# Kernel tuning notes

Hardware: AMD Instinct MI355X
Metric: run time of the kernel (lower is better)

Reference implementation:

```python
import jax, jax.numpy as jnp
import numpy as np
from jax import lax

LONG_EDGE = 1024
MAX_SIZE = 1333.0
STRIDES = (4, 8, 16, 32, 64)
SIZES = (32, 64, 128, 256, 512)
RATIOS = (0.5, 1.0, 2.0)
PRE_NMS_TOPK = 6000
POST_NMS_TOPK = 1000
NMS_THRESH = 0.7
NUM_CH = 256


def _gen_anchors_level(scale, ratios, shape, stride):
    # faithful copy of generate_anchors_keras (numpy, static)
    scales, ratios = np.meshgrid(np.array([scale], dtype=np.float64), np.array(ratios, dtype=np.float64))
    scales = scales.flatten(); ratios = ratios.flatten()
    size_ratios = stride * stride / ratios
    widths = np.round(np.sqrt(size_ratios))
    heights = np.round(widths * ratios)
    widths = widths * (scales / stride)
    heights = heights * (scales / stride)
    shifts_y = np.arange(0, shape[0]) * stride + (stride - 1) / 2
    shifts_x = np.arange(0, shape[1]) * stride + (stride - 1) / 2
    shifts_x, shifts_y = np.meshgrid(shifts_x, shifts_y)
    box_widths, box_centers_x = np.meshgrid(widths, shifts_x)
    box_heights, box_centers_y = np.meshgrid(heights, shifts_y)
    box_centers = np.stack([box_centers_y, box_centers_x], axis=2).reshape([-1, 2])
    box_sizes = np.stack([box_heights, box_widths], axis=2).reshape([-1, 2])
    boxes = np.concatenate([box_centers - 0.5 * (box_sizes - 1), box_centers + 0.5 * (box_sizes - 1)], axis=1)
    boxes[:, [2, 3]] += 1
    return boxes[:, [1, 0, 3, 2]].astype(np.float32)


def all_anchors():
    shapes = [(int(np.ceil(LONG_EDGE / s)),) * 2 for s in STRIDES]
    return np.concatenate([_gen_anchors_level(SIZES[i], RATIOS, shapes[i], STRIDES[i]) for i in range(len(STRIDES))], axis=0)


def conv2d(x, w, b, padding):
    y = lax.conv_general_dilated(x, w, (1, 1), padding, dimension_numbers=('NCHW', 'OIHW', 'NCHW'))
    return y + b[None, :, None, None]


def decode_bbox_target(deltas, anchors):
    # deltas, anchors: [K,4]
    txty, twth = deltas[:, :2], deltas[:, 2:]
    x1y1, x2y2 = anchors[:, :2], anchors[:, 2:]
    waha = x2y2 - x1y1
    xaya = (x2y2 + x1y1) * 0.5
    clipv = jnp.float32(np.log(MAX_SIZE / 16.0))
    wbhb = jnp.exp(jnp.minimum(twth, clipv)) * waha
    xbyb = txty * waha + xaya
    return jnp.concatenate([xbyb - wbhb * 0.5, xbyb + wbhb * 0.5], axis=1)


def clip_boxes(b, h, w):
    # faithful to source: x clamped to window[0]=h, y to window[1]=w
    return jnp.stack([b[:, 0].clip(0.0, h), b[:, 1].clip(0.0, w), b[:, 2].clip(0.0, h), b[:, 3].clip(0.0, w)], 1)


def nms_keep(boxes, thresh):
    # boxes sorted by descending score; greedy NMS over full IoU matrix
    x1, y1, x2, y2 = boxes[:, 0], boxes[:, 1], boxes[:, 2], boxes[:, 3]
    areas = (x2 - x1) * (y2 - y1)
    iw = jnp.clip(jnp.minimum(x2[:, None], x2[None, :]) - jnp.maximum(x1[:, None], x1[None, :]), 0.0)
    ih = jnp.clip(jnp.minimum(y2[:, None], y2[None, :]) - jnp.maximum(y1[:, None], y1[None, :]), 0.0)
    inter = iw * ih
    iou = inter / (areas[:, None] + areas[None, :] - inter)
    n = boxes.shape[0]
    sup = iou > thresh
    idxs = jnp.arange(n)
    def body(i, keep):
        row = sup[i] & (idxs > i)
        return jnp.where(keep[i], keep & ~row, keep)
    return lax.fori_loop(0, n, body, jnp.ones((n,), bool))


def rpn_forward(image, feats, w0, b0, wcls, bcls, wbox, bbox):
    labels, boxes_l = [], []
    for f in feats:
        hidden = jax.nn.relu(conv2d(f, w0, b0, 'SAME'))
        cls = conv2d(hidden, wcls, bcls, 'VALID')   # [1,A,H,W]
        box = conv2d(hidden, wbox, bbox, 'VALID')   # [1,4A,H,W]
        labels.append(jnp.transpose(cls, (0, 2, 3, 1)).reshape(1, -1, 1))
        boxes_l.append(jnp.transpose(box, (0, 2, 3, 1)).reshape(1, -1, 4))
    scores = jnp.concatenate(labels, axis=1)[0, :, 0]          # [N]
    box_logits = jnp.concatenate(boxes_l, axis=1)[0]           # [N,4]
    anchors = jnp.asarray(all_anchors())                       # [N,4]
    k = min(PRE_NMS_TOPK, anchors.shape[0])
    _, order = lax.top_k(scores, k)
    deltas = box_logits[order]
    pre_anch = anchors[order]
    dec = decode_bbox_target(deltas, pre_anch)
    h, w = float(image.shape[2]), float(image.shape[3])
    boxes = clip_boxes(dec, h, w)
    keep = nms_keep(lax.stop_gradient(boxes), NMS_THRESH)
    sel = jnp.argsort(~keep)[:POST_NMS_TOPK]  # stable: kept boxes in score order, then pad slots
    proposals = jnp.where(keep[sel][:, None], boxes[sel], 0.0)
    return proposals


def setup_inputs() -> dict:
    key = jax.random.key(0)
    ks = jax.random.split(key, 9)
    hw = [256, 128, 64, 32, 16]
    inp = {'image': jax.random.normal(ks[0], (1, 3, 1024, 1024), jnp.float32)}
    for i, s in enumerate(hw):
        inp[f'feat{i}'] = jax.random.normal(jax.random.fold_in(ks[1], i), (1, NUM_CH, s, s), jnp.float32)
    inp['w0'] = jax.random.normal(ks[2], (NUM_CH, NUM_CH, 3, 3), jnp.float32) * 0.01
    inp['b0'] = jnp.zeros((NUM_CH,), jnp.float32)
    inp['wcls'] = jax.random.normal(ks[3], (3, NUM_CH, 1, 1), jnp.float32) * 0.01
    inp['bcls'] = jnp.zeros((3,), jnp.float32)
    inp['wbox'] = jax.random.normal(ks[4], (12, NUM_CH, 1, 1), jnp.float32) * 0.01
    inp['bbox'] = jnp.zeros((12,), jnp.float32)
    return inp


def reference(image, feat0, feat1, feat2, feat3, feat4, w0, b0, wcls, bcls, wbox, bbox):
    feats = [feat0, feat1, feat2, feat3, feat4]
    return rpn_forward(image, feats, w0, b0, wcls, bcls, wbox, bbox)
```

## Files before the change

### kernel.cpp

```cpp
#include <hip/hip_runtime.h>
#include <cstdint>

typedef unsigned long long u64;
typedef unsigned int u32;
typedef unsigned short ushort;
typedef __attribute__((ext_vector_type(8))) short short8;
typedef __attribute__((ext_vector_type(4))) float f32x4;

#define A_TOTAL 261888
#define NPIX    87296
#define KTOP    6000
#define KTARGET 7800
#define NWORDS  94
#define CANDMAX 8192
#define PIXMAX  8192
#define NBINS   16384

__device__ __forceinline__ u64 score_key64(double s) {
  u64 u = (u64)__double_as_longlong(s);
  return (u & 0x8000000000000000ULL) ? ~u : (u | 0x8000000000000000ULL);
}
__device__ __forceinline__ u32 key32(float s) {
  u32 u = __float_as_uint(s);
  return (u & 0x80000000u) ? ~u : (u | 0x80000000u);
}
__device__ __forceinline__ ushort f2bf(float f) {
  u32 u = __float_as_uint(f);
  u32 r = (u + 0x7FFFu + ((u >> 16) & 1u)) >> 16;
  return (ushort)r;
}
__device__ __forceinline__ void pix_level(int pix, int& l, int& off) {
  if (pix < 65536)      { l = 0; off = 0; }
  else if (pix < 81920) { l = 1; off = 65536; }
  else if (pix < 86016) { l = 2; off = 81920; }
  else if (pix < 87040) { l = 3; off = 86016; }
  else                  { l = 4; off = 87040; }
}

__global__ void k_prep_w(const float* __restrict__ w0, float* __restrict__ wt,
                         ushort* __restrict__ wkf) {
  int i = blockIdx.x * 256 + threadIdx.x;
  if (i < 256 * 2304) {
    int o = i & 255;
    int ictap = i >> 8;
    float v = w0[o * 2304 + ictap];
    wt[ictap * 256 + o] = v;
    int ic = ictap / 9;
    int tap = ictap - ic * 9;
    int w = o >> 6, mt = (o >> 4) & 3, l15 = o & 15;
    int ch = ic >> 5, kk = ic & 31;
    int l4 = kk >> 3, e = kk & 7;
    int lane = l4 * 16 + l15;
    wkf[((((w * 4 + mt) * 8 + ch) * 9 + tap) << 9) + lane * 8 + e] = f2bf(v);
  }
}

__global__ __launch_bounds__(256, 2) void k_conv_mfma(
    const float* __restrict__ f0, const float* __restrict__ f1,
    const float* __restrict__ f2, const float* __restrict__ f3,
    const float* __restrict__ f4,
    const ushort* __restrict__ wkf, const float* __restrict__ b0,
    const float* __restrict__ wcls, const float* __restrict__ bcls,
    float* __restrict__ scr)
{
  __shared__ ushort xsl[100][40];
  __shared__ float  part[3][64][17];

  int b = blockIdx.x;
  int l, tb;
  if (b < 1024)      { l = 0; tb = b; }
  else if (b < 1280) { l = 1; tb = b - 1024; }
  else if (b < 1344) { l = 2; tb = b - 1280; }
  else if (b < 1360) { l = 3; tb = b - 1344; }
  else               { l = 4; tb = b - 1360; }
  const float* feat = (l == 0) ? f0 : (l == 1) ? f1 : (l == 2) ? f2 : (l == 3) ? f3 : f4;
  int Hh = 256 >> l;
  int HW = Hh * Hh;
  int pixOff = (l == 0) ? 0 : (l == 1) ? 65536 : (l == 2) ? 81920 : (l == 3) ? 86016 : 87040;
  int shl = 5 - l;
  int ty = (tb >> shl) << 3;
  int tx = (tb & ((1 << shl) - 1)) << 3;

  int tid = threadIdx.x;
  int w = tid >> 6;
  int lane = tid & 63;
  int l15 = lane & 15;
  int l4 = lane >> 4;

  f32x4 zz = {0.f, 0.f, 0.f, 0.f};
  f32x4 acc[4][4];
  #pragma unroll
  for (int mt = 0; mt < 4; ++mt)
    #pragma unroll
    for (int tt = 0; tt < 4; ++tt) acc[mt][tt] = zz;

  for (int ch = 0; ch < 8; ++ch) {
    __syncthreads();
    for (int e = tid; e < 3200; e += 256) {
      int icl = e / 100;
      int sp = e - icl * 100;
      int yy = sp / 10;
      int xx = sp - yy * 10;
      int gy = ty + yy - 1, gx = tx + xx - 1;
      float v = 0.f;
      if (gy >= 0 && gy < Hh && gx >= 0 && gx < Hh)
        v = feat[(ch * 32 + icl) * HW + gy * Hh + gx];
      xsl[sp][icl] = f2bf(v);
    }
    __syncthreads();
    #pragma unroll
    for (int tap = 0; tap < 9; ++tap) {
      int dy = tap / 3;
      int dx = tap - dy * 3;
      short8 af[4], bf[4];
      #pragma unroll
      for (int mt = 0; mt < 4; ++mt) {
        int abase = ((((w * 4 + mt) * 8 + ch) * 9 + tap) << 9) + (lane << 3);
        af[mt] = *(const short8*)(wkf + abase);
      }
      #pragma unroll
      for (int tt = 0; tt < 4; ++tt) {
        int p = (tt << 4) + l15;
        int sp = ((p >> 3) + dy) * 10 + (p & 7) + dx;
        bf[tt] = *(const short8*)&xsl[sp][l4 << 3];
      }
      #pragma unroll
      for (int mt = 0; mt < 4; ++mt)
        #pragma unroll
        for (int tt = 0; tt < 4; ++tt)
          acc[mt][tt] = __builtin_amdgcn_mfma_f32_16x16x32_bf16(af[mt], bf[tt], acc[mt][tt], 0, 0, 0);
    }
  }

  float pr[3][4];
  #pragma unroll
  for (int kk = 0; kk < 3; ++kk)
    #pragma unroll
    for (int tt = 0; tt < 4; ++tt) pr[kk][tt] = 0.f;
  #pragma unroll
  for (int mt = 0; mt < 4; ++mt) {
    #pragma unroll
    for (int r = 0; r < 4; ++r) {
      int oc = (w << 6) + (mt << 4) + (l4 << 2) + r;
      float bb = b0[oc];
      float c0 = wcls[oc], c1 = wcls[256 + oc], c2 = wcls[512 + oc];
      #pragma unroll
      for (int tt = 0; tt < 4; ++tt) {
        float v = acc[mt][tt][r] + bb;
        v = v > 0.f ? v : 0.f;
        pr[0][tt] = fmaf(c0, v, pr[0][tt]);
        pr[1][tt] = fmaf(c1, v, pr[1][tt]);
        pr[2][tt] = fmaf(c2, v, pr[2][tt]);
      }
    }
  }
  __syncthreads();
  #pragma unroll
  for (int kk = 0; kk < 3; ++kk)
    #pragma unroll
    for (int tt = 0; tt < 4; ++tt)
      part[kk][(tt << 4) + l15][(w << 2) + l4] = pr[kk][tt];
  __syncthreads();
  if (tid < 192) {
    int kk = tid >> 6;
    int px = tid & 63;
    float s = 0.f;
    #pragma unroll
    for (int q = 0; q < 16; ++q) s += part[kk][px][q];
    int pix = pixOff + (ty + (px >> 3)) * Hh + (tx + (px & 7));
    scr[pix * 3 + kk] = s + bcls[kk];
  }
}

__global__ void k_hist1(const float* __restrict__ scr, u32* __restrict__ bins) {
  __shared__ u32 h[NBINS];
  int tid = threadIdx.x;
  for (int idx = tid; idx < NBINS; idx += 256) h[idx] = 0;
  __syncthreads();
  for (int i = blockIdx.x * 256 + tid; i < A_TOTAL; i += gridDim.x * 256)
    atomicAdd(&h[key32(scr[i]) >> 18], 1u);
  __syncthreads();
  for (int idx = tid; idx < NBINS; idx += 256) {
    u32 v = h[idx];
    if (v) atomicAdd(&bins[idx], v);
  }
}

__global__ void k_scan1(const u32* __restrict__ bins, u32* __restrict__ meta) {
  __shared__ u32 psum[256];
  int tid = threadIdx.x;
  u32 s = 0;
  for (int u = 0; u < 64; ++u) s += bins[tid * 64 + u];
  psum[tid] = s;
  __syncthreads();
  if (tid == 0) {
    u32 run = 0;
    for (int t = 255; t >= 0; --t) { u32 tmp = psum[t]; psum[t] = run; run += tmp; }
  }
  __syncthreads();
  u32 cum = psum[tid];
  if (cum < (u32)KTARGET) {
    for (int u = 63; u >= 0; --u) {
      u32 bv = bins[tid * 64 + u];
      u32 nc = cum + bv;
      if (nc >= (u32)KTARGET) {
        meta[0] = (u32)(tid * 64 + u);
        meta[2] = cum;
        break;
      }
      cum = nc;
    }
  }
}

__global__ void k_hist2(const float* __restrict__ scr, const u32* __restrict__ meta,
                        u32* __restrict__ sub) {
  int i = blockIdx.x * 256 + threadIdx.x;
  if (i < A_TOTAL) {
    u32 k = key32(scr[i]);
    if ((k >> 18) == meta[0]) atomicAdd(&sub[(k >> 10) & 0xFFu], 1u);
  }
}

__global__ void k_scan2(const u32* __restrict__ sub, u32* __restrict__ meta) {
  if (threadIdx.x == 0) {
    u32 b = meta[0];
    u32 c = meta[2];
    u32 T = b << 18;
    for (int u = 255; u >= 0; --u) {
      c += sub[u];
      if (c >= (u32)KTARGET) { T = (b << 18) | ((u32)u << 10); break; }
    }
    meta[3] = (T >= (2u << 10)) ? (T - (2u << 10)) : 0u;
  }
}

__global__ void k_cnt(const float* __restrict__ scr, const u32* __restrict__ meta,
                      u32* __restrict__ blkCnt) {
  __shared__ u32 wc[4];
  int tid = threadIdx.x;
  int i = blockIdx.x * 256 + tid;
  bool q = (i < A_TOTAL) && (key32(scr[i]) >= meta[3]);
  u64 b = __ballot(q);
  if ((tid & 63) == 0) wc[tid >> 6] = (u32)__popcll(b);
  __syncthreads();
  if (tid == 0) blkCnt[blockIdx.x] = wc[0] + wc[1] + wc[2] + wc[3];
}

__global__ __launch_bounds__(1024) void k_scanblk(const u32* __restrict__ blkCnt,
                                                  u32* __restrict__ blkOff,
                                                  u32* __restrict__ totalOut) {
  __shared__ u32 buf[2][1024];
  int tid = threadIdx.x;
  u32 v = (tid < 1023) ? blkCnt[tid] : 0u;
  buf[0][tid] = v;
  __syncthreads();
  int src = 0;
  for (int d = 1; d < 1024; d <<= 1) {
    u32 t = buf[src][tid] + ((tid >= d) ? buf[src][tid - d] : 0u);
    buf[src ^ 1][tid] = t;
    src ^= 1;
    __syncthreads();
  }
  if (tid < 1023) blkOff[tid] = buf[src][tid] - v;
  if (tid == 0) totalOut[0] = buf[src][1022];
}

__global__ void k_fill(const float* __restrict__ scr, const u32* __restrict__ meta,
                       const u32* __restrict__ blkOff, u32* __restrict__ candIdx) {
  __shared__ u32 wbase[4];
  int tid = threadIdx.x;
  int lane = tid & 63, wv = tid >> 6;
  int i = blockIdx.x * 256 + tid;
  bool q = (i < A_TOTAL) && (key32(scr[i]) >= meta[3]);
  u64 b = __ballot(q);
  if (lane == 0) wbase[wv] = (u32)__popcll(b);
  __syncthreads();
  if (tid == 0) {
    u32 r = blkOff[blockIdx.x];
    #pragma unroll
    for (int w2 = 0; w2 < 4; ++w2) { u32 t = wbase[w2]; wbase[w2] = r; r += t; }
  }
  __syncthreads();
  if (q) {
    u32 rank = (u32)__popcll(b & ((1ULL << lane) - 1ULL));
    u32 pos = wbase[wv] + rank;
    if (pos < CANDMAX) candIdx[pos] = (u32)i;
  }
}

__global__ void k_cntP(const float* __restrict__ scr, const u32* __restrict__ meta,
                       u32* __restrict__ blkCntP) {
  __shared__ u32 wc[4];
  int tid = threadIdx.x;
  int p = blockIdx.x * 256 + tid;
  bool q = false;
  if (p < NPIX) {
    u32 T = meta[3];
    q = (key32(scr[p * 3 + 0]) >= T) || (key32(scr[p * 3 + 1]) >= T) || (key32(scr[p * 3 + 2]) >= T);
  }
  u64 b = __ballot(q);
  if ((tid & 63) == 0) wc[tid >> 6] = (u32)__popcll(b);
  __syncthreads();
  if (tid == 0) blkCntP[blockIdx.x] = wc[0] + wc[1] + wc[2] + wc[3];
}

__global__ void k_fillP(const float* __restrict__ scr, const u32* __restrict__ meta,
                        const u32* __restrict__ blkOffP,
                        u32* __restrict__ pixList, u32* __restrict__ pixMap) {
  __shared__ u32 wbase[4];
  int tid = threadIdx.x;
  int lane = tid & 63, wv = tid >> 6;
  int p = blockIdx.x * 256 + tid;
  bool q = false;
  if (p < NPIX) {
    u32 T = meta[3];
    q = (key32(scr[p * 3 + 0]) >= T) || (key32(scr[p * 3 + 1]) >= T) || (key32(scr[p * 3 + 2]) >= T);
  }
  u64 b = __ballot(q);
  if (lane == 0) wbase[wv] = (u32)__popcll(b);
  __syncthreads();
  if (tid == 0) {
    u32 r = blkOffP[blockIdx.x];
    #pragma unroll
    for (int w2 = 0; w2 < 4; ++w2) { u32 t = wbase[w2]; wbase[w2] = r; r += t; }
  }
  __syncthreads();
  if (q) {
    u32 rank = (u32)__popcll(b & ((1ULL << lane) - 1ULL));
    u32 pos = wbase[wv] + rank;
    if (pos < PIXMAX) { pixList[pos] = (u32)p; pixMap[p] = pos; }
  }
}

#define KC 576
__global__ __launch_bounds__(256, 4) void k_hidden(
    const float* __restrict__ f0, const float* __restrict__ f1,
    const float* __restrict__ f2, const float* __restrict__ f3,
    const float* __restrict__ f4,
    const float* __restrict__ wt, const float* __restrict__ b0,
    const u32* __restrict__ pixList, const u32* __restrict__ meta,
    double* __restrict__ hbuf)
{
  __shared__ __align__(16) float patch[2][KC][8];
  __shared__ int sValid[8], sY[8], sX[8], sW[8], sL[8];

  int tid = threadIdx.x;
  int base = blockIdx.x * 8;
  u32 np = meta[4];
  if (np > PIXMAX) np = PIXMAX;
  if (base >= (int)np) return;

  if (tid < 8) {
    int slot = base + tid;
    int v = slot < (int)np;
    sValid[tid] = v;
    int pix = v ? (int)pixList[slot] : 0;
    int l, off;
    pix_level(pix, l, off);
    int W = 256 >> l;
    int idx = pix - off;
    sL[tid] = l;
    sW[tid] = W;
    sY[tid] = idx >> (8 - l);
    sX[tid] = idx & (W - 1);
  }
  __syncthreads();

  auto stage = [&](int c, int pb) {
    for (int t = tid; t < 1536; t += 256) {
      int s = t / 192;
      int rem = t - s * 192;
      int icl = rem / 3;
      int dy = rem - icl * 3;
      int ic = c * 64 + icl;
      float v0 = 0.f, v1 = 0.f, v2 = 0.f;
      if (sValid[s]) {
        int l = sL[s], W = sW[s], y = sY[s], x = sX[s];
        const float* feat = (l == 0) ? f0 : (l == 1) ? f1 : (l == 2) ? f2 : (l == 3) ? f3 : f4;
        int gy = y + dy - 1;
        if (gy >= 0 && gy < W) {
          const float* rowp = feat + ic * W * W + gy * W;
          if (x - 1 >= 0) v0 = rowp[x - 1];
          v1 = rowp[x];
          if (x + 1 < W) v2 = rowp[x + 1];
        }
      }
      int kb = icl * 9 + dy * 3;
      patch[pb][kb + 0][s] = v0;
      patch[pb][kb + 1][s] = v1;
      patch[pb][kb + 2][s] = v2;
    }
  };

  stage(0, 0);
  __syncthreads();

  double h[8];
  #pragma unroll
  for (int s = 0; s < 8; ++s) h[s] = 0.0;

  for (int c = 0; c < 4; ++c) {
    if (c < 3) stage(c + 1, (c + 1) & 1);
    const float* wcol = wt + (c * KC) * 256 + tid;
    const float (*pc)[8] = patch[c & 1];
    for (int kk = 0; kk < KC; ++kk) {
      double wv_ = (double)wcol[(size_t)kk * 256];
      float4 pa = *(const float4*)&pc[kk][0];
      float4 pb2 = *(const float4*)&pc[kk][4];
      h[0] = fma(wv_, (double)pa.x, h[0]);
      h[1] = fma(wv_, (double)pa.y, h[1]);
      h[2] = fma(wv_, (double)pa.z, h[2]);
      h[3] = fma(wv_, (double)pa.w, h[3]);
      h[4] = fma(wv_, (double)pb2.x, h[4]);
      h[5] = fma(wv_, (double)pb2.y, h[5]);
      h[6] = fma(wv_, (double)pb2.z, h[6]);
      h[7] = fma(wv_, (double)pb2.w, h[7]);
    }
    __syncthreads();
  }

  double bb = (double)b0[tid];
  #pragma unroll
  for (int s = 0; s < 8; ++s) {
    if (sValid[s]) {
      double t = h[s] + bb;
      hbuf[(size_t)(base + s) * 256 + tid] = t > 0.0 ? t : 0.0;
    }
  }
}

__global__ __launch_bounds__(256, 4) void k_heads(
    const float* __restrict__ wcls, const float* __restrict__ bcls,
    const float* __restrict__ wbox, const float* __restrict__ bbox,
    const u32* __restrict__ candIdx, const u32* __restrict__ pixMap,
    const u32* __restrict__ meta, const double* __restrict__ hbuf,
    u64* __restrict__ candKey, u32* __restrict__ candPack, double* __restrict__ candDelta)
{
  __shared__ double wavePart[8][5][4];
  __shared__ int sIdx[8], sValid[8], sR[8], sPS[8];
  int tid = threadIdx.x;
  int lane = tid & 63;
  int wv = tid >> 6;
  int base = blockIdx.x * 8;
  u32 cnt = meta[1];
  if (cnt > CANDMAX) cnt = CANDMAX;

  if (base >= (int)cnt) {
    if (tid < 8) {
      candKey[base + tid] = 0ULL;
      candPack[base + tid] = 0xFFFFFFFFu;
    }
    return;
  }

  if (tid < 8) {
    int slot = base + tid;
    int v = slot < (int)cnt;
    sValid[tid] = v;
    int aidx = v ? (int)candIdx[slot] : 0;
    sIdx[tid] = aidx;
    int pix = aidx / 3;
    sR[tid] = aidx - pix * 3;
    sPS[tid] = v ? (int)pixMap[pix] : 0;
  }
  __syncthreads();

  for (int s = 0; s < 8; ++s) {
    if (!sValid[s]) continue;
    int r = sR[s];
    double hv = hbuf[(size_t)sPS[s] * 256 + tid];
    double p0 = (double)wcls[r * 256 + tid] * hv;
    double p1 = (double)wbox[(r * 4 + 0) * 256 + tid] * hv;
    double p2 = (double)wbox[(r * 4 + 1) * 256 + tid] * hv;
    double p3 = (double)wbox[(r * 4 + 2) * 256 + tid] * hv;
    double p4 = (double)wbox[(r * 4 + 3) * 256 + tid] * hv;
    #pragma unroll
    for (int d = 32; d; d >>= 1) {
      p0 += __shfl_xor(p0, d);
      p1 += __shfl_xor(p1, d);
      p2 += __shfl_xor(p2, d);
      p3 += __shfl_xor(p3, d);
      p4 += __shfl_xor(p4, d);
    }
    if (lane == 0) {
      wavePart[s][0][wv] = p0;
      wavePart[s][1][wv] = p1;
      wavePart[s][2][wv] = p2;
      wavePart[s][3][wv] = p3;
      wavePart[s][4][wv] = p4;
    }
  }
  __syncthreads();
  if (tid < 40) {
    int s = tid / 5;
    int k = tid - s * 5;
    int slot = base + s;
    if (sValid[s]) {
      double v = wavePart[s][k][0] + wavePart[s][k][1] + wavePart[s][k][2] + wavePart[s][k][3];
      int r = sR[s];
      if (k == 0) {
        double sc_ = v + (double)bcls[r];
        candKey[slot] = score_key64(sc_);
        candPack[slot] = ((u32)sIdx[s] << 13) | (u32)slot;
      } else {
        candDelta[(size_t)slot * 4 + (k - 1)] = v + (double)bbox[r * 4 + (k - 1)];
      }
    } else if (k == 0) {
      candKey[slot] = 0ULL;
      candPack[slot] = 0xFFFFFFFFu;
    }
  }
}

__global__ __launch_bounds__(256) void k_rank(const u64* __restrict__ candKey,
                                              const u32* __restrict__ candPack,
                                              u32* __restrict__ order) {
  __shared__ u64 fk[1024];
  __shared__ u32 fp[1024];
  __shared__ u32 rsum[32][8];
  int tid = threadIdx.x;
  int c = tid & 31;
  int g = tid >> 5;
  int ci = blockIdx.x * 32 + c;
  u64 mk = candKey[ci];
  u32 mp = candPack[ci];
  u32 cnt = 0;
  for (int chunk = 0; chunk < 8; ++chunk) {
    __syncthreads();
    for (int e = tid; e < 1024; e += 256) {
      fk[e] = candKey[chunk * 1024 + e];
      fp[e] = candPack[chunk * 1024 + e];
    }
    __syncthreads();
    int j0 = g * 128;
    #pragma unroll 4
    for (int j = j0; j < j0 + 128; ++j) {
      u64 kj = fk[j];
      cnt += (kj > mk || (kj == mk && fp[j] < mp)) ? 1u : 0u;
    }
  }
  rsum[c][g] = cnt;
  __syncthreads();
  if (tid < 32) {
    u32 rank = 0;
    #pragma unroll
    for (int q = 0; q < 8; ++q) rank += rsum[tid][q];
    if (rank < (u32)KTOP) order[rank] = mp;
  }
}

__global__ void k_decode(const u32* __restrict__ order, const double* __restrict__ candDelta,
                         double* __restrict__ boxesD) {
  int i = blockIdx.x * 64 + threadIdx.x;
  if (i >= KTOP) return;
  u32 pack = order[i];
  u32 slot = pack & 0x1FFFu;
  u32 a = pack >> 13;
  int pix = (int)(a / 3u);
  int r = (int)(a - (u32)pix * 3u);
  int l, off;
  pix_level(pix, l, off);
  int W = 256 >> l;
  int idx = pix - off;
  int y = idx >> (8 - l);
  int x = idx & (W - 1);
  int s = 4 << l;
  double ratio = (r == 0) ? 0.5 : (r == 1) ? 1.0 : 2.0;
  double wq = rint(sqrt((double)(s * s) / ratio));
  double hq = rint(wq * ratio);
  double Wa = wq * 8.0, Ha = hq * 8.0;
  double cx = (double)x * (double)s + (double)(s - 1) * 0.5;
  double cy = (double)y * (double)s + (double)(s - 1) * 0.5;
  double ax1 = (double)(float)(cx - 0.5 * (Wa - 1.0));
  double ay1 = (double)(float)(cy - 0.5 * (Ha - 1.0));
  double ax2 = (double)(float)(cx + 0.5 * (Wa - 1.0) + 1.0);
  double ay2 = (double)(float)(cy + 0.5 * (Ha - 1.0) + 1.0);
  double tx = candDelta[(size_t)slot * 4 + 0], tyv = candDelta[(size_t)slot * 4 + 1];
  double tw = candDelta[(size_t)slot * 4 + 2], th  = candDelta[(size_t)slot * 4 + 3];
  double wa = ax2 - ax1, ha = ay2 - ay1;
  double xa = (ax1 + ax2) * 0.5, ya = (ay1 + ay2) * 0.5;
  double clipv = (double)(float)log(1333.0 / 16.0);
  double wb = exp(fmin(tw, clipv)) * wa;
  double hb = exp(fmin(th, clipv)) * ha;
  double xb = tx * wa + xa;
  double yb = tyv * ha + ya;
  double bx1 = xb - 0.5 * wb, by1 = yb - 0.5 * hb;
  double bx2 = xb + 0.5 * wb, by2 = yb + 0.5 * hb;
  bx1 = fmin(fmax(bx1, 0.0), 1024.0);
  by1 = fmin(fmax(by1, 0.0), 1024.0);
  bx2 = fmin(fmax(bx2, 0.0), 1024.0);
  by2 = fmin(fmax(by2, 0.0), 1024.0);
  boxesD[(size_t)i * 4 + 0] = bx1;
  boxesD[(size_t)i * 4 + 1] = by1;
  boxesD[(size_t)i * 4 + 2] = bx2;
  boxesD[(size_t)i * 4 + 3] = by2;
}

__global__ void k_mask(const double* __restrict__ boxesD, u64* __restrict__ maskA) {
  __shared__ double cbx[64][4];
  int lane = threadIdx.x;
  int bc = blockIdx.x, br = blockIdx.y;
  if (bc < br) return;
  int ci = bc * 64 + lane;
  if (ci < KTOP) {
    cbx[lane][0] = boxesD[(size_t)ci * 4 + 0];
    cbx[lane][1] = boxesD[(size_t)ci * 4 + 1];
    cbx[lane][2] = boxesD[(size_t)ci * 4 + 2];
    cbx[lane][3] = boxesD[(size_t)ci * 4 + 3];
  } else {
    cbx[lane][0] = -1e30; cbx[lane][1] = -1e30; cbx[lane][2] = -1e30; cbx[lane][3] = -1e30;
  }
  __syncthreads();
  int ri = br * 64 + lane;
  if (ri >= KTOP) return;
  double rx1 = boxesD[(size_t)ri * 4 + 0], ry1 = boxesD[(size_t)ri * 4 + 1];
  double rx2 = boxesD[(size_t)ri * 4 + 2], ry2 = boxesD[(size_t)ri * 4 + 3];
  double ra = (rx2 - rx1) * (ry2 - ry1);
  u64 bits = 0;
  #pragma unroll 4
  for (int j = 0; j < 64; ++j) {
    int cj = bc * 64 + j;
    double iw = fmin(rx2, cbx[j][2]) - fmax(rx1, cbx[j][0]);
    double ih = fmin(ry2, cbx[j][3]) - fmax(ry1, cbx[j][1]);
    iw = fmax(iw, 0.0); ih = fmax(ih, 0.0);
    double inter = iw * ih;
    double ca = (cbx[j][2] - cbx[j][0]) * (cbx[j][3] - cbx[j][1]);
    double iou = inter / (ra + ca - inter);
    if (cj > ri && iou > 0.7) bits |= (1ULL << j);
  }
  maskA[(size_t)ri * NWORDS + bc] = bits;
}

__global__ __launch_bounds__(1024) void k_nms_reduce(const u64* __restrict__ maskA,
                                                     u32* __restrict__ keep) {
  __shared__ u64 rm[NWORDS];
  int tid = threadIdx.x;
  int wv = tid >> 6, lane = tid & 63;
  for (int i = tid; i < NWORDS; i += 1024) rm[i] = 0ULL;
  __syncthreads();
  u64 diagNext = maskA[(size_t)lane * NWORDS + 0];
  int keptTot = 0;
  for (int c = 0; c < NWORDS; ++c) {
    int rows = KTOP - c * 64; if (rows > 64) rows = 64;
    u64 validM = (rows == 64) ? ~0ULL : ((1ULL << rows) - 1ULL);
    size_t rowbase = (size_t)(c * 64 + lane) * NWORDS;
    bool lv = lane < rows;
    int w0i = c + wv;
    u64 v0 = (lv && w0i      < NWORDS) ? maskA[rowbase + w0i]      : 0ULL;
    u64 v1 = (lv && w0i + 16 < NWORDS) ? maskA[rowbase + w0i + 16] : 0ULL;
    u64 v2 = (lv && w0i + 32 < NWORDS) ? maskA[rowbase + w0i + 32] : 0ULL;
    u64 v3 = (lv && w0i + 48 < NWORDS) ? maskA[rowbase + w0i + 48] : 0ULL;
    u64 v4 = (lv && w0i + 64 < NWORDS) ? maskA[rowbase + w0i + 64] : 0ULL;
    u64 v5 = (lv && w0i + 80 < NWORDS) ? maskA[rowbase + w0i + 80] : 0ULL;
    u64 diag = diagNext;
    if (c + 1 < NWORDS) {
      int nrows = KTOP - (c + 1) * 64; if (nrows > 64) nrows = 64;
      diagNext = (lane < nrows) ? maskA[(size_t)((c + 1) * 64 + lane) * NWORDS + (c + 1)] : 0ULL;
    }
    u64 R = rm[c];
    u64 undec = (~R) & validM;
    u64 km = 0;
    while (undec) {
      int j = __builtin_ctzll(undec);
      km |= (1ULL << j);
      u64 dj = (u64)__shfl((unsigned long long)diag, j);
      undec &= ~(dj | (1ULL << j));
    }
    if (wv == 0 && lane < rows) keep[c * 64 + lane] = (u32)((km >> lane) & 1ULL);
    keptTot += (int)__popcll(km);
    if (keptTot >= 1000) {
      for (int i = (c + 1) * 64 + tid; i < KTOP; i += 1024) keep[i] = 0u;
      return;
    }
    u64 sel = ((km >> lane) & 1ULL) ? ~0ULL : 0ULL;
    v0 &= sel; v1 &= sel; v2 &= sel; v3 &= sel; v4 &= sel; v5 &= sel;
    #pragma unroll
    for (int s = 32; s; s >>= 1) {
      v0 |= (u64)__shfl_xor((unsigned long long)v0, s);
      v1 |= (u64)__shfl_xor((unsigned long long)v1, s);
      v2 |= (u64)__shfl_xor((unsigned long long)v2, s);
      v3 |= (u64)__shfl_xor((unsigned long long)v3, s);
      v4 |= (u64)__shfl_xor((unsigned long long)v4, s);
      v5 |= (u64)__shfl_xor((unsigned long long)v5, s);
    }
    if (lane == 0) {
      if (w0i      < NWORDS) rm[w0i]      |= v0;
      if (w0i + 16 < NWORDS) rm[w0i + 16] |= v1;
      if (w0i + 32 < NWORDS) rm[w0i + 32] |= v2;
      if (w0i + 48 < NWORDS) rm[w0i + 48] |= v3;
      if (w0i + 64 < NWORDS) rm[w0i + 64] |= v4;
      if (w0i + 80 < NWORDS) rm[w0i + 80] |= v5;
    }
    __syncthreads();
  }
}

__global__ __launch_bounds__(1024) void k_emit(const u32* __restrict__ keep,
                                               const double* __restrict__ boxesD,
                                               float* __restrict__ out) {
  __shared__ u32 partial[1024];
  __shared__ u32 excl[1024];
  int tid = threadIdx.x;
  for (int j = tid; j < 4000; j += 1024) out[j] = 0.f;
  int base = tid * 6;
  u32 kv[6];
  u32 c = 0;
  #pragma unroll
  for (int u = 0; u < 6; ++u) {
    int j = base + u;
    kv[u] = (j < KTOP) ? keep[j] : 0u;
    c += kv[u];
  }
  partial[tid] = c;
  __syncthreads();
  if (tid == 0) {
    u32 run = 0;
    for (int t = 0; t < 1024; ++t) { excl[t] = run; run += partial[t]; }
  }
  __syncthreads();
  u32 p = excl[tid];
  #pragma unroll
  for (int u = 0; u < 6; ++u) {
    int j = base + u;
    if (j < KTOP && kv[u]) {
      if (p < 1000u) {
        out[p * 4 + 0] = (float)boxesD[(size_t)j * 4 + 0];
        out[p * 4 + 1] = (float)boxesD[(size_t)j * 4 + 1];
        out[p * 4 + 2] = (float)boxesD[(size_t)j * 4 + 2];
        out[p * 4 + 3] = (float)boxesD[(size_t)j * 4 + 3];
      }
      ++p;
    }
  }
}

extern "C" void kernel_launch(void* const* d_in, const int* in_sizes, int n_in,
                              void* d_out, int out_size, void* d_ws, size_t ws_size,
                              hipStream_t stream) {
  const float* f0   = (const float*)d_in[1];
  const float* f1   = (const float*)d_in[2];
  const float* f2   = (const float*)d_in[3];
  const float* f3   = (const float*)d_in[4];
  const float* f4   = (const float*)d_in[5];
  const float* w0   = (const float*)d_in[6];
  const float* b0   = (const float*)d_in[7];
  const float* wcls = (const float*)d_in[8];
  const float* bcls = (const float*)d_in[9];
  const float* wbox = (const float*)d_in[10];
  const float* bbox = (const float*)d_in[11];
  float* out = (float*)d_out;
  char* ws = (char*)d_ws;

  size_t off = 0;
  auto alloc = [&](size_t bytes) { size_t o = off; off += (bytes + 255) & ~(size_t)255; return o; };
  size_t off_scr  = alloc((size_t)A_TOTAL * 4);
  size_t off_wt   = alloc((size_t)256 * 2304 * 4);
  size_t off_wk   = alloc((size_t)256 * 2304 * 2);
  size_t off_hb   = alloc((size_t)PIXMAX * 256 * 8);
  size_t off_ci   = alloc((size_t)CANDMAX * 4);
  size_t off_ck   = alloc((size_t)CANDMAX * 8);
  size_t off_cp   = alloc((size_t)CANDMAX * 4);
  size_t off_cd   = alloc((size_t)CANDMAX * 4 * 8);
  size_t off_pl   = alloc((size_t)PIXMAX * 4);
  size_t off_pm   = alloc((size_t)NPIX * 4);
  size_t off_box  = alloc((size_t)KTOP * 4 * 8);
  size_t off_ord  = alloc((size_t)KTOP * 4);
  size_t off_keep = alloc((size_t)KTOP * 4);
  size_t off_mask = alloc((size_t)KTOP * NWORDS * 8);
  size_t off_bcnt = alloc((size_t)1024 * 4);
  size_t off_boff = alloc((size_t)1024 * 4);
  size_t off_bcp  = alloc((size_t)1024 * 4);
  size_t off_bop  = alloc((size_t)1024 * 4);
  size_t off_bins = alloc((size_t)NBINS * 4);
  size_t off_sub  = alloc((size_t)256 * 4);
  size_t off_meta = alloc((size_t)64 * 4);
  size_t off_end  = off;
  (void)in_sizes; (void)n_in; (void)out_size; (void)ws_size;

  float*  scr       = (float*)(ws + off_scr);
  float*  wt        = (float*)(ws + off_wt);
  ushort* wkf       = (ushort*)(ws + off_wk);
  double* hbuf      = (double*)(ws + off_hb);
  u32*    candIdx   = (u32*)(ws + off_ci);
  u64*    candKey   = (u64*)(ws + off_ck);
  u32*    candPack  = (u32*)(ws + off_cp);
  double* candDelta = (double*)(ws + off_cd);
  u32*    pixList   = (u32*)(ws + off_pl);
  u32*    pixMap    = (u32*)(ws + off_pm);
  double* boxesD    = (double*)(ws + off_box);
  u32*    order     = (u32*)(ws + off_ord);
  u32*    keep      = (u32*)(ws + off_keep);
  u64*    maskA     = (u64*)(ws + off_mask);
  u32*    blkCnt    = (u32*)(ws + off_bcnt);
  u32*    blkOff    = (u32*)(ws + off_boff);
  u32*    blkCntP   = (u32*)(ws + off_bcp);
  u32*    blkOffP   = (u32*)(ws + off_bop);
  u32*    bins      = (u32*)(ws + off_bins);
  u32*    sub       = (u32*)(ws + off_sub);
  u32*    meta      = (u32*)(ws + off_meta);

  hipMemsetAsync(ws + off_bins, 0, off_end - off_bins, stream);

  k_prep_w<<<2304, 256, 0, stream>>>(w0, wt, wkf);
  k_conv_mfma<<<1364, 256, 0, stream>>>(f0, f1, f2, f3, f4, wkf, b0, wcls, bcls, scr);
  k_hist1<<<64, 256, 0, stream>>>(scr, bins);
  k_scan1<<<1, 256, 0, stream>>>(bins, meta);
  k_hist2<<<1023, 256, 0, stream>>>(scr, meta, sub);
  k_scan2<<<1, 64, 0, stream>>>(sub, meta);
  k_cnt<<<1023, 256, 0, stream>>>(scr, meta, blkCnt);
  k_scanblk<<<1, 1024, 0, stream>>>(blkCnt, blkOff, meta + 1);
  k_fill<<<1023, 256, 0, stream>>>(scr, meta, blkOff, candIdx);
  k_cntP<<<1023, 256, 0, stream>>>(scr, meta, blkCntP);
  k_scanblk<<<1, 1024, 0, stream>>>(blkCntP, blkOffP, meta + 4);
  k_fillP<<<1023, 256, 0, stream>>>(scr, meta, blkOffP, pixList, pixMap);
  k_hidden<<<PIXMAX / 8, 256, 0, stream>>>(f0, f1, f2, f3, f4, wt, b0, pixList, meta, hbuf);
  k_heads<<<CANDMAX / 8, 256, 0, stream>>>(wcls, bcls, wbox, bbox, candIdx, pixMap, meta, hbuf,
                                           candKey, candPack, candDelta);
  k_rank<<<CANDMAX / 32, 256, 0, stream>>>(candKey, candPack, order);
  k_decode<<<94, 64, 0, stream>>>(order, candDelta, boxesD);
  k_mask<<<dim3(NWORDS, NWORDS), 64, 0, stream>>>(boxesD, maskA);
  k_nms_reduce<<<1, 1024, 0, stream>>>(maskA, keep);
  k_emit<<<1, 1024, 0, stream>>>(keep, boxesD, out);
}
```

Baseline: 981.3 us.

## Recompute selected hidden pixels with FP64 MFMA and fuse compaction passes

```diff
diff --git a/kernel.cpp b/kernel.cpp
--- a/kernel.cpp
+++ b/kernel.cpp
@@ -6,6 +6,7 @@
 typedef unsigned short ushort;
 typedef __attribute__((ext_vector_type(8))) short short8;
 typedef __attribute__((ext_vector_type(4))) float f32x4;
+typedef __attribute__((ext_vector_type(4))) double f64x4;
 
 #define A_TOTAL 261888
 #define NPIX    87296
@@ -16,6 +17,15 @@
 #define PIXMAX  8192
 #define NBINS   16384
 
+#if defined(__has_builtin)
+#if __has_builtin(__builtin_amdgcn_mfma_f64_16x16x4f64)
+#define HAVE_DGEMM 1
+#endif
+#endif
+#ifndef HAVE_DGEMM
+#define HAVE_DGEMM 0
+#endif
+
 __device__ __forceinline__ u64 score_key64(double s) {
   u64 u = (u64)__double_as_longlong(s);
   return (u & 0x8000000000000000ULL) ? ~u : (u | 0x8000000000000000ULL);
@@ -37,14 +47,14 @@
   else                  { l = 4; off = 87040; }
 }
 
-__global__ void k_prep_w(const float* __restrict__ w0, float* __restrict__ wt,
+__global__ void k_prep_w(const float* __restrict__ w0, double* __restrict__ wt64,
                          ushort* __restrict__ wkf) {
   int i = blockIdx.x * 256 + threadIdx.x;
   if (i < 256 * 2304) {
     int o = i & 255;
     int ictap = i >> 8;
     float v = w0[o * 2304 + ictap];
-    wt[ictap * 256 + o] = v;
+    wt64[(size_t)ictap * 256 + o] = (double)v;
     int ic = ictap / 9;
     int tap = ictap - ic * 9;
     int w = o >> 6, mt = (o >> 4) & 3, l15 = o & 15;
@@ -53,6 +63,30 @@
     int lane = l4 * 16 + l15;
     wkf[((((w * 4 + mt) * 8 + ch) * 9 + tap) << 9) + lane * 8 + e] = f2bf(v);
   }
+}
+
+__global__ void k_probe(u32* __restrict__ flag) {
+#if HAVE_DGEMM
+  int l = threadIdx.x;
+  int m = l & 15, kq = l >> 4;
+  double a = (double)(1 + m * 4 + kq);
+  double b = (double)(1 + m * 4 + kq * 67);
+  f64x4 c = {0.0, 0.0, 0.0, 0.0};
+  c = __builtin_amdgcn_mfma_f64_16x16x4f64(a, b, c, 0, 0, 0);
+  bool ok = true;
+  #pragma unroll
+  for (int r = 0; r < 4; ++r) {
+    int row = 4 * kq + r, col = m;
+    double e = 0.0;
+    for (int k = 0; k < 4; ++k)
+      e += (double)(1 + row * 4 + k) * (double)(1 + col * 4 + k * 67);
+    if (c[r] != e) ok = false;
+  }
+  u64 bal = __ballot(ok);
+  if (l == 0) *flag = (bal == ~0ULL) ? 1u : 0u;
+#else
+  if (threadIdx.x == 0) *flag = 0u;
+#endif
 }
 
 __global__ __launch_bounds__(256, 2) void k_conv_mfma(
@@ -235,115 +269,203 @@
   }
 }
 
-__global__ void k_cnt(const float* __restrict__ scr, const u32* __restrict__ meta,
-                      u32* __restrict__ blkCnt) {
-  __shared__ u32 wc[4];
-  int tid = threadIdx.x;
+__global__ void k_cnt2(const float* __restrict__ scr, const u32* __restrict__ meta,
+                       u32* __restrict__ blkCnt, u32* __restrict__ blkCntP) {
+  __shared__ u32 wc[4], wcp[4];
+  int tid = threadIdx.x;
+  int lane = tid & 63, wv = tid >> 6;
+  u32 T = meta[3];
   int i = blockIdx.x * 256 + tid;
-  bool q = (i < A_TOTAL) && (key32(scr[i]) >= meta[3]);
-  u64 b = __ballot(q);
-  if ((tid & 63) == 0) wc[tid >> 6] = (u32)__popcll(b);
-  __syncthreads();
-  if (tid == 0) blkCnt[blockIdx.x] = wc[0] + wc[1] + wc[2] + wc[3];
-}
-
-__global__ __launch_bounds__(1024) void k_scanblk(const u32* __restrict__ blkCnt,
-                                                  u32* __restrict__ blkOff,
-                                                  u32* __restrict__ totalOut) {
+  bool qa = (i < A_TOTAL) && (key32(scr[i]) >= T);
+  u64 ba = __ballot(qa);
+  bool qp = false;
+  if (i < NPIX)
+    qp = (key32(scr[i * 3 + 0]) >= T) || (key32(scr[i * 3 + 1]) >= T) || (key32(scr[i * 3 + 2]) >= T);
+  u64 bp = __ballot(qp);
+  if (lane == 0) { wc[wv] = (u32)__popcll(ba); wcp[wv] = (u32)__popcll(bp); }
+  __syncthreads();
+  if (tid == 0) {
+    blkCnt[blockIdx.x]  = wc[0] + wc[1] + wc[2] + wc[3];
+    blkCntP[blockIdx.x] = wcp[0] + wcp[1] + wcp[2] + wcp[3];
+  }
+}
+
+__global__ __launch_bounds__(1024) void k_scanblk2(const u32* __restrict__ blkCnt,
+                                                   u32* __restrict__ blkOff,
+                                                   u32* __restrict__ totA,
+                                                   const u32* __restrict__ blkCntP,
+                                                   u32* __restrict__ blkOffP,
+                                                   u32* __restrict__ totP) {
   __shared__ u32 buf[2][1024];
   int tid = threadIdx.x;
-  u32 v = (tid < 1023) ? blkCnt[tid] : 0u;
-  buf[0][tid] = v;
-  __syncthreads();
-  int src = 0;
-  for (int d = 1; d < 1024; d <<= 1) {
-    u32 t = buf[src][tid] + ((tid >= d) ? buf[src][tid - d] : 0u);
-    buf[src ^ 1][tid] = t;
-    src ^= 1;
+  for (int pass = 0; pass < 2; ++pass) {
+    const u32* src_ = pass ? blkCntP : blkCnt;
+    u32* dst_ = pass ? blkOffP : blkOff;
+    u32* tot_ = pass ? totP : totA;
+    u32 v = (tid < 1023) ? src_[tid] : 0u;
+    buf[0][tid] = v;
     __syncthreads();
-  }
-  if (tid < 1023) blkOff[tid] = buf[src][tid] - v;
-  if (tid == 0) totalOut[0] = buf[src][1022];
-}
-
-__global__ void k_fill(const float* __restrict__ scr, const u32* __restrict__ meta,
-                       const u32* __restrict__ blkOff, u32* __restrict__ candIdx) {
-  __shared__ u32 wbase[4];
+    int src = 0;
+    for (int d = 1; d < 1024; d <<= 1) {
+      u32 t = buf[src][tid] + ((tid >= d) ? buf[src][tid - d] : 0u);
+      buf[src ^ 1][tid] = t;
+      src ^= 1;
+      __syncthreads();
+    }
+    if (tid < 1023) dst_[tid] = buf[src][tid] - v;
+    if (tid == 0) tot_[0] = buf[src][1022];
+    __syncthreads();
+  }
+}
+
+__global__ void k_fill2(const float* __restrict__ scr, const u32* __restrict__ meta,
+                        const u32* __restrict__ blkOff, const u32* __restrict__ blkOffP,
+                        u32* __restrict__ candIdx, u32* __restrict__ pixList,
+                        u32* __restrict__ pixMap) {
+  __shared__ u32 wbase[4], wbaseP[4];
   int tid = threadIdx.x;
   int lane = tid & 63, wv = tid >> 6;
+  u32 T = meta[3];
   int i = blockIdx.x * 256 + tid;
-  bool q = (i < A_TOTAL) && (key32(scr[i]) >= meta[3]);
-  u64 b = __ballot(q);
-  if (lane == 0) wbase[wv] = (u32)__popcll(b);
+  bool qa = (i < A_TOTAL) && (key32(scr[i]) >= T);
+  u64 ba = __ballot(qa);
+  bool qp = false;
+  if (i < NPIX)
+    qp = (key32(scr[i * 3 + 0]) >= T) || (key32(scr[i * 3 + 1]) >= T) || (key32(scr[i * 3 + 2]) >= T);
+  u64 bp = __ballot(qp);
+  if (lane == 0) { wbase[wv] = (u32)__popcll(ba); wbaseP[wv] = (u32)__popcll(bp); }
   __syncthreads();
   if (tid == 0) {
     u32 r = blkOff[blockIdx.x];
     #pragma unroll
     for (int w2 = 0; w2 < 4; ++w2) { u32 t = wbase[w2]; wbase[w2] = r; r += t; }
-  }
-  __syncthreads();
-  if (q) {
-    u32 rank = (u32)__popcll(b & ((1ULL << lane) - 1ULL));
+    u32 rp = blkOffP[blockIdx.x];
+    #pragma unroll
+    for (int w2 = 0; w2 < 4; ++w2) { u32 t = wbaseP[w2]; wbaseP[w2] = rp; rp += t; }
+  }
+  __syncthreads();
+  if (qa) {
+    u32 rank = (u32)__popcll(ba & ((1ULL << lane) - 1ULL));
     u32 pos = wbase[wv] + rank;
     if (pos < CANDMAX) candIdx[pos] = (u32)i;
   }
-}
-
-__global__ void k_cntP(const float* __restrict__ scr, const u32* __restrict__ meta,
-                       u32* __restrict__ blkCntP) {
-  __shared__ u32 wc[4];
-  int tid = threadIdx.x;
-  int p = blockIdx.x * 256 + tid;
-  bool q = false;
-  if (p < NPIX) {
-    u32 T = meta[3];
-    q = (key32(scr[p * 3 + 0]) >= T) || (key32(scr[p * 3 + 1]) >= T) || (key32(scr[p * 3 + 2]) >= T);
-  }
-  u64 b = __ballot(q);
-  if ((tid & 63) == 0) wc[tid >> 6] = (u32)__popcll(b);
-  __syncthreads();
-  if (tid == 0) blkCntP[blockIdx.x] = wc[0] + wc[1] + wc[2] + wc[3];
-}
-
-__global__ void k_fillP(const float* __restrict__ scr, const u32* __restrict__ meta,
-                        const u32* __restrict__ blkOffP,
-                        u32* __restrict__ pixList, u32* __restrict__ pixMap) {
-  __shared__ u32 wbase[4];
-  int tid = threadIdx.x;
-  int lane = tid & 63, wv = tid >> 6;
-  int p = blockIdx.x * 256 + tid;
-  bool q = false;
-  if (p < NPIX) {
-    u32 T = meta[3];
-    q = (key32(scr[p * 3 + 0]) >= T) || (key32(scr[p * 3 + 1]) >= T) || (key32(scr[p * 3 + 2]) >= T);
-  }
-  u64 b = __ballot(q);
-  if (lane == 0) wbase[wv] = (u32)__popcll(b);
-  __syncthreads();
-  if (tid == 0) {
-    u32 r = blkOffP[blockIdx.x];
-    #pragma unroll
-    for (int w2 = 0; w2 < 4; ++w2) { u32 t = wbase[w2]; wbase[w2] = r; r += t; }
-  }
-  __syncthreads();
-  if (q) {
-    u32 rank = (u32)__popcll(b & ((1ULL << lane) - 1ULL));
-    u32 pos = wbase[wv] + rank;
-    if (pos < PIXMAX) { pixList[pos] = (u32)p; pixMap[p] = pos; }
-  }
-}
-
-#define KC 576
-__global__ __launch_bounds__(256, 4) void k_hidden(
+  if (qp) {
+    u32 rank = (u32)__popcll(bp & ((1ULL << lane) - 1ULL));
+    u32 pos = wbaseP[wv] + rank;
+    if (pos < PIXMAX) { pixList[pos] = (u32)i; pixMap[i] = pos; }
+  }
+}
+
+#define KCH 288
+__global__ __launch_bounds__(256, 3) void k_hidden_mfma(
     const float* __restrict__ f0, const float* __restrict__ f1,
     const float* __restrict__ f2, const float* __restrict__ f3,
     const float* __restrict__ f4,
-    const float* __restrict__ wt, const float* __restrict__ b0,
+    const double* __restrict__ wt64, const float* __restrict__ b0,
+    const u32* __restrict__ pixList, const u32* __restrict__ meta,
+    double* __restrict__ hbuf)
+{
+#if HAVE_DGEMM
+  __shared__ float patch[2][KCH][16];
+  __shared__ int sValid[16], sY[16], sX[16], sW[16], sL[16];
+  if (meta[8] == 0) return;
+  int tid = threadIdx.x;
+  int base = blockIdx.x * 16;
+  u32 np = meta[4];
+  if (np > PIXMAX) np = PIXMAX;
+  if (base >= (int)np) return;
+
+  if (tid < 16) {
+    int slot = base + tid;
+    int v = slot < (int)np;
+    sValid[tid] = v;
+    int pix = v ? (int)pixList[slot] : 0;
+    int l, off;
+    pix_level(pix, l, off);
+    int W = 256 >> l;
+    int idx = pix - off;
+    sL[tid] = l;
+    sW[tid] = W;
+    sY[tid] = idx >> (8 - l);
+    sX[tid] = idx & (W - 1);
+  }
+  __syncthreads();
+
+  auto stage = [&](int cb, int pb) {
+    for (int t = tid; t < 1536; t += 256) {
+      int s = t & 15;
+      int rem = t >> 4;
+      int icl = rem / 3;
+      int dy = rem - icl * 3;
+      int ic = cb * 32 + icl;
+      float v0 = 0.f, v1 = 0.f, v2 = 0.f;
+      if (sValid[s]) {
+        int l = sL[s], W = sW[s], y = sY[s], x = sX[s];
+        const float* feat = (l == 0) ? f0 : (l == 1) ? f1 : (l == 2) ? f2 : (l == 3) ? f3 : f4;
+        int gy = y + dy - 1;
+        if (gy >= 0 && gy < W) {
+          const float* rowp = feat + ic * W * W + gy * W;
+          if (x - 1 >= 0) v0 = rowp[x - 1];
+          v1 = rowp[x];
+          if (x + 1 < W) v2 = rowp[x + 1];
+        }
+      }
+      int kb = icl * 9 + dy * 3;
+      patch[pb][kb + 0][s] = v0;
+      patch[pb][kb + 1][s] = v1;
+      patch[pb][kb + 2][s] = v2;
+    }
+  };
+
+  int lane = tid & 63, w = tid >> 6;
+  int m = lane & 15, kq = lane >> 4;
+  f64x4 acc[4];
+  #pragma unroll
+  for (int mt = 0; mt < 4; ++mt) acc[mt] = f64x4{0.0, 0.0, 0.0, 0.0};
+
+  stage(0, 0);
+  __syncthreads();
+  for (int cb = 0; cb < 8; ++cb) {
+    if (cb < 7) stage(cb + 1, (cb + 1) & 1);
+    const float (*pc)[16] = patch[cb & 1];
+    for (int ks = 0; ks < KCH / 4; ++ks) {
+      double bv = (double)pc[ks * 4 + kq][m];
+      const double* wr = wt64 + (size_t)(cb * KCH + ks * 4 + kq) * 256 + w * 64 + m;
+      #pragma unroll
+      for (int mt = 0; mt < 4; ++mt)
+        acc[mt] = __builtin_amdgcn_mfma_f64_16x16x4f64(wr[mt * 16], bv, acc[mt], 0, 0, 0);
+    }
+    __syncthreads();
+  }
+
+  int slot = base + m;
+  bool pv = sValid[m];
+  #pragma unroll
+  for (int mt = 0; mt < 4; ++mt) {
+    #pragma unroll
+    for (int r = 0; r < 4; ++r) {
+      int oc = w * 64 + mt * 16 + 4 * kq + r;
+      if (pv) {
+        double t2 = acc[mt][r] + (double)b0[oc];
+        hbuf[(size_t)slot * 256 + oc] = t2 > 0.0 ? t2 : 0.0;
+      }
+    }
+  }
+#endif
+}
+
+#define KC 576
+__global__ __launch_bounds__(256, 4) void k_hidden_valu(
+    const float* __restrict__ f0, const float* __restrict__ f1,
+    const float* __restrict__ f2, const float* __restrict__ f3,
+    const float* __restrict__ f4,
+    const double* __restrict__ wt64, const float* __restrict__ b0,
     const u32* __restrict__ pixList, const u32* __restrict__ meta,
     double* __restrict__ hbuf)
 {
   __shared__ __align__(16) float patch[2][KC][8];
   __shared__ int sValid[8], sY[8], sX[8], sW[8], sL[8];
+  if (meta[8] != 0) return;
 
   int tid = threadIdx.x;
   int base = blockIdx.x * 8;
@@ -402,10 +524,10 @@
 
   for (int c = 0; c < 4; ++c) {
     if (c < 3) stage(c + 1, (c + 1) & 1);
-    const float* wcol = wt + (c * KC) * 256 + tid;
+    const double* wcol = wt64 + (size_t)(c * KC) * 256 + tid;
     const float (*pc)[8] = patch[c & 1];
     for (int kk = 0; kk < KC; ++kk) {
-      double wv_ = (double)wcol[(size_t)kk * 256];
+      double wv_ = wcol[(size_t)kk * 256];
       float4 pa = *(const float4*)&pc[kk][0];
       float4 pb2 = *(const float4*)&pc[kk][4];
       h[0] = fma(wv_, (double)pa.x, h[0]);
@@ -755,7 +877,7 @@
   size_t off = 0;
   auto alloc = [&](size_t bytes) { size_t o = off; off += (bytes + 255) & ~(size_t)255; return o; };
   size_t off_scr  = alloc((size_t)A_TOTAL * 4);
-  size_t off_wt   = alloc((size_t)256 * 2304 * 4);
+  size_t off_w64  = alloc((size_t)256 * 2304 * 8);
   size_t off_wk   = alloc((size_t)256 * 2304 * 2);
   size_t off_hb   = alloc((size_t)PIXMAX * 256 * 8);
   size_t off_ci   = alloc((size_t)CANDMAX * 4);
@@ -779,7 +901,7 @@
   (void)in_sizes; (void)n_in; (void)out_size; (void)ws_size;
 
   float*  scr       = (float*)(ws + off_scr);
-  float*  wt        = (float*)(ws + off_wt);
+  double* wt64      = (double*)(ws + off_w64);
   ushort* wkf       = (ushort*)(ws + off_wk);
   double* hbuf      = (double*)(ws + off_hb);
   u32*    candIdx   = (u32*)(ws + off_ci);
@@ -802,19 +924,18 @@
 
   hipMemsetAsync(ws + off_bins, 0, off_end - off_bins, stream);
 
-  k_prep_w<<<2304, 256, 0, stream>>>(w0, wt, wkf);
+  k_prep_w<<<2304, 256, 0, stream>>>(w0, wt64, wkf);
+  k_probe<<<1, 64, 0, stream>>>(meta + 8);
   k_conv_mfma<<<1364, 256, 0, stream>>>(f0, f1, f2, f3, f4, wkf, b0, wcls, bcls, scr);
   k_hist1<<<64, 256, 0, stream>>>(scr, bins);
   k_scan1<<<1, 256, 0, stream>>>(bins, meta);
   k_hist2<<<1023, 256, 0, stream>>>(scr, meta, sub);
   k_scan2<<<1, 64, 0, stream>>>(sub, meta);
-  k_cnt<<<1023, 256, 0, stream>>>(scr, meta, blkCnt);
-  k_scanblk<<<1, 1024, 0, stream>>>(blkCnt, blkOff, meta + 1);
-  k_fill<<<1023, 256, 0, stream>>>(scr, meta, blkOff, candIdx);
-  k_cntP<<<1023, 256, 0, stream>>>(scr, meta, blkCntP);
-  k_scanblk<<<1, 1024, 0, stream>>>(blkCntP, blkOffP, meta + 4);
-  k_fillP<<<1023, 256, 0, stream>>>(scr, meta, blkOffP, pixList, pixMap);
-  k_hidden<<<PIXMAX / 8, 256, 0, stream>>>(f0, f1, f2, f3, f4, wt, b0, pixList, meta, hbuf);
+  k_cnt2<<<1023, 256, 0, stream>>>(scr, meta, blkCnt, blkCntP);
+  k_scanblk2<<<1, 1024, 0, stream>>>(blkCnt, blkOff, meta + 1, blkCntP, blkOffP, meta + 4);
+  k_fill2<<<1023, 256, 0, stream>>>(scr, meta, blkOff, blkOffP, candIdx, pixList, pixMap);
+  k_hidden_mfma<<<PIXMAX / 16, 256, 0, stream>>>(f0, f1, f2, f3, f4, wt64, b0, pixList, meta, hbuf);
+  k_hidden_valu<<<PIXMAX / 8, 256, 0, stream>>>(f0, f1, f2, f3, f4, wt64, b0, pixList, meta, hbuf);
   k_heads<<<CANDMAX / 8, 256, 0, stream>>>(wcls, bcls, wbox, bbox, candIdx, pixMap, meta, hbuf,
                                            candKey, candPack, candDelta);
   k_rank<<<CANDMAX / 32, 256, 0, stream>>>(candKey, candPack, order);
```

Result: no change. 983.7 us (+0.2%).
